# Kernel tuning notes

Measured on AMD Instinct MI355X. Metric: run time of the kernel, lower is better.

Reference implementation:

```python
import jax, jax.numpy as jnp
import numpy as np

N_NODES = 100000
IN_F = 512
OUT_F = 512
N_EDGES = 3200000


def setup_inputs() -> dict:
    key = jax.random.key(0)
    k1, k2, k3, k4, k5 = jax.random.split(key, 5)
    features = jax.random.normal(k1, (N_NODES, IN_F), dtype=jnp.float32)
    # xavier_uniform: bound = sqrt(6/(in+out))
    bound = np.sqrt(6.0 / (IN_F + OUT_F)).astype(np.float32)
    weight = jax.random.uniform(k2, (IN_F, OUT_F), dtype=jnp.float32,
                                minval=-bound, maxval=bound)
    edge_row = jax.random.randint(k3, (N_EDGES,), 0, N_NODES, dtype=jnp.int32)
    edge_col = jax.random.randint(k4, (N_EDGES,), 0, N_NODES, dtype=jnp.int32)
    # normalized-adjacency-like positive values
    edge_val = jax.random.uniform(k5, (N_EDGES,), dtype=jnp.float32)
    return {"features": features, "weight": weight, "edge_row": edge_row,
            "edge_col": edge_col, "edge_val": edge_val}


def reference(features, weight, edge_row, edge_col, edge_val):
    # support = features @ W   (dense GEMM, [N, out])
    support = features @ weight
    # output = spmm(adj, support): out[r] += val * support[c] for each edge (r, c)
    messages = edge_val[:, None] * support[edge_col]          # [E, out]
    output = jax.ops.segment_sum(messages, edge_row, num_segments=N_NODES)
    # active=True branch: fused ReLU
    return jax.nn.relu(output)
```

## Files before the change

### kernel.cpp

```cpp
#include <hip/hip_runtime.h>
#include <hip/hip_bf16.h>

#define N_NODES 100000
#define M_PAD   100096
#define FDIM    512
#define N_EDGES 3200000
#define GEMM_BLOCKS 3128
#define GEMM_MAIN   3104

#define NB    782
#define B1    782
#define SLICE 4096

typedef __attribute__((ext_vector_type(8))) short short8;
typedef __attribute__((ext_vector_type(8))) unsigned short ushort8;
typedef __attribute__((ext_vector_type(4))) float floatx4;
typedef __attribute__((ext_vector_type(2))) int intx2;

__device__ __forceinline__ unsigned short f2bf(float f) {
    unsigned u = __float_as_uint(f);
    u += 0x7FFFu + ((u >> 16) & 1u);
    return (unsigned short)(u >> 16);
}
__device__ __forceinline__ float bf2f(unsigned short u) {
    return __uint_as_float(((unsigned)u) << 16);
}

__global__ __launch_bounds__(256) void convert_w_k(const float* __restrict__ W,
                                                   unsigned short* __restrict__ Wt) {
    int idx = blockIdx.x * 256 + threadIdx.x;
    int k = idx >> 9, n = idx & 511;
    Wt[n * 512 + k] = f2bf(W[idx]);
}

__global__ __launch_bounds__(256) void convert_a_k(const float* __restrict__ F,
                                                   unsigned short* __restrict__ Af) {
    int i = blockIdx.x * 256 + threadIdx.x;
    if (i >= (N_NODES * FDIM) / 8) return;
    const float4* p = (const float4*)F + (size_t)i * 2;
    float4 a = p[0], b = p[1];
    ushort8 u = { f2bf(a.x), f2bf(a.y), f2bf(a.z), f2bf(a.w),
                  f2bf(b.x), f2bf(b.y), f2bf(b.z), f2bf(b.w) };
    *(ushort8*)(Af + (size_t)i * 8) = u;
}

__global__ __launch_bounds__(256) void hist1_k(const int* __restrict__ row,
                                               int* __restrict__ H) {
    __shared__ int h[NB];
    const int b = blockIdx.x;
    for (int k = threadIdx.x; k < NB; k += 256) h[k] = 0;
    __syncthreads();
    const int base = b * SLICE;
    const int limit = min(base + SLICE, N_EDGES);
    for (int i = base + threadIdx.x; i < limit; i += 256)
        atomicAdd(&h[row[i] >> 7], 1);
    __syncthreads();
    for (int k = threadIdx.x; k < NB; k += 256)
        H[b * NB + k] = h[k];
}

__global__ __launch_bounds__(1024) void scanA_k(int* __restrict__ H,
                                                int* __restrict__ totals) {
    __shared__ int sm[1024];
    const int k = blockIdx.x, tid = threadIdx.x;
    int v = (tid < B1) ? H[tid * NB + k] : 0;
    sm[tid] = v;
    __syncthreads();
    #pragma unroll
    for (int off = 1; off < 1024; off <<= 1) {
        int t = (tid >= off) ? sm[tid - off] : 0;
        __syncthreads();
        sm[tid] += t;
        __syncthreads();
    }
    if (tid < B1) H[tid * NB + k] = sm[tid] - v;
    if (tid == B1 - 1) totals[k] = sm[tid];
}

__global__ __launch_bounds__(1024) void scanB_k(const int* __restrict__ totals,
                                                int* __restrict__ start) {
    __shared__ int sm[1024];
    const int tid = threadIdx.x;
    int v = (tid < NB) ? totals[tid] : 0;
    sm[tid] = v;
    __syncthreads();
    #pragma unroll
    for (int off = 1; off < 1024; off <<= 1) {
        int t = (tid >= off) ? sm[tid - off] : 0;
        __syncthreads();
        sm[tid] += t;
        __syncthreads();
    }
    if (tid < NB) start[tid] = sm[tid] - v;
    if (tid == 0) start[NB] = N_EDGES;
}

__global__ __launch_bounds__(256) void scatter1_k(const int* __restrict__ row,
                                                  const int* __restrict__ col,
                                                  const float* __restrict__ val,
                                                  const int* __restrict__ H,
                                                  const int* __restrict__ start,
                                                  int2* __restrict__ tmp_cv,
                                                  unsigned char* __restrict__ tmp_r8) {
    __shared__ int cur[NB];
    const int b = blockIdx.x;
    for (int k = threadIdx.x; k < NB; k += 256)
        cur[k] = start[k] + H[b * NB + k];
    __syncthreads();
    const int base = b * SLICE;
    const int limit = min(base + SLICE, N_EDGES);
    for (int i = base + threadIdx.x; i < limit; i += 256) {
        int r = row[i];
        int p = atomicAdd(&cur[r >> 7], 1);
        tmp_cv[p] = make_int2(col[i], __float_as_int(val[i]));
        tmp_r8[p] = (unsigned char)(r & 127);
    }
}

__global__ __launch_bounds__(256) void sort2_k(const int* __restrict__ start,
                                               const int2* __restrict__ tmp_cv,
                                               const unsigned char* __restrict__ tmp_r8,
                                               int* __restrict__ row_start,
                                               int2* __restrict__ edges) {
    __shared__ int h[128];
    __shared__ int cur[128];
    const int k = blockIdx.x, tid = threadIdx.x;
    const int base = start[k], cnt = start[k + 1] - base;
    if (tid < 128) h[tid] = 0;
    __syncthreads();
    for (int i = tid; i < cnt; i += 256)
        atomicAdd(&h[tmp_r8[base + i]], 1);
    __syncthreads();
    int v = (tid < 128) ? h[tid] : 0;
    #pragma unroll
    for (int off = 1; off < 128; off <<= 1) {
        int t = (tid >= off && tid < 128) ? h[tid - off] : 0;
        __syncthreads();
        if (tid < 128) h[tid] += t;
        __syncthreads();
    }
    if (tid < 128) {
        int excl = h[tid] - v;
        int r = (k << 7) + tid;
        if (r < N_NODES) row_start[r] = base + excl;
        cur[tid] = base + excl;
    }
    if (k == NB - 1 && tid == 0) row_start[N_NODES] = N_EDGES;
    __syncthreads();
    for (int i = tid; i < cnt; i += 256) {
        unsigned char rl = tmp_r8[base + i];
        int p = atomicAdd(&cur[rl], 1);
        edges[p] = tmp_cv[base + i];
    }
}

__global__ __launch_bounds__(256) void gemm_k(const unsigned short* __restrict__ A,
                                              const unsigned short* __restrict__ Bt,
                                              unsigned short* __restrict__ C) {
    const int id = blockIdx.x;
    int mb, nb;
    if (id < GEMM_MAIN) {
        mb = (id >> 5) * 8 + (id & 7);
        nb = (id >> 3) & 3;
    } else {
        int t = id - GEMM_MAIN;
        mb = 776 + (t >> 2);
        nb = t & 3;
    }
    const int baseM = mb * 128;
    const int baseN = nb * 128;
    const int tid  = threadIdx.x;
    const int lane = tid & 63, wave = tid >> 6;
    const int wm = (wave & 1) * 64;
    const int wn = (wave >> 1) * 64;
    const int lrow = lane & 15, quad = lane >> 4;

    __shared__ unsigned short As[128 * 64];
    __shared__ unsigned short Bs[128 * 64];

    floatx4 acc[4][4] = {};

    for (int k0 = 0; k0 < FDIM; k0 += 64) {
        #pragma unroll
        for (int i = 0; i < 4; ++i) {
            int ofs = i * 4096 + tid * 16;
            int row = ofs >> 7;
            int ke  = (ofs & 127) >> 1;
            __builtin_amdgcn_global_load_lds(
                (const __attribute__((address_space(1))) void*)
                    (A + (size_t)(baseM + row) * FDIM + k0 + ke),
                (__attribute__((address_space(3))) void*)((char*)As + ofs),
                16, 0, 0);
            __builtin_amdgcn_global_load_lds(
                (const __attribute__((address_space(1))) void*)
                    (Bt + (size_t)(baseN + row) * FDIM + k0 + ke),
                (__attribute__((address_space(3))) void*)((char*)Bs + ofs),
                16, 0, 0);
        }
        __syncthreads();

        short8 af[4][2], bfr[4][2];
        #pragma unroll
        for (int mi = 0; mi < 4; ++mi)
            #pragma unroll
            for (int kk = 0; kk < 2; ++kk)
                af[mi][kk] = *(const short8*)(As + (wm + mi * 16 + lrow) * 64 + kk * 32 + quad * 8);
        #pragma unroll
        for (int ni = 0; ni < 4; ++ni)
            #pragma unroll
            for (int kk = 0; kk < 2; ++kk)
                bfr[ni][kk] = *(const short8*)(Bs + (wn + ni * 16 + lrow) * 64 + kk * 32 + quad * 8);
        #pragma unroll
        for (int kk = 0; kk < 2; ++kk)
            #pragma unroll
            for (int mi = 0; mi < 4; ++mi)
                #pragma unroll
                for (int ni = 0; ni < 4; ++ni)
                    acc[mi][ni] = __builtin_amdgcn_mfma_f32_16x16x32_bf16(
                        af[mi][kk], bfr[ni][kk], acc[mi][ni], 0, 0, 0);
        __syncthreads();
    }

    #pragma unroll
    for (int mi = 0; mi < 4; ++mi)
        #pragma unroll
        for (int ni = 0; ni < 4; ++ni)
            #pragma unroll
            for (int rr = 0; rr < 4; ++rr) {
                int row  = baseM + wm + mi * 16 + quad * 4 + rr;
                int colj = baseN + wn + ni * 16 + lrow;
                if (row < N_NODES)
                    C[(size_t)row * FDIM + colj] = f2bf(acc[mi][ni][rr]);
            }
}

__global__ __launch_bounds__(256) void spmm_k(const unsigned short* __restrict__ sup,
                                              const int* __restrict__ row_start,
                                              const int2* __restrict__ edges,
                                              float* __restrict__ out) {
    const int r = blockIdx.x * 4 + (threadIdx.x >> 6);
    const int lane = threadIdx.x & 63;
    const int start = row_start[r], end = row_start[r + 1];
    const unsigned short* supl = sup + lane * 8;

    float acc[8] = {0.f, 0.f, 0.f, 0.f, 0.f, 0.f, 0.f, 0.f};

    const int n8 = (end - start) & ~7;
    for (int eb = start; eb < start + n8; eb += 8) {
        intx2 p[8];
        #pragma unroll
        for (int j = 0; j < 8; ++j)
            p[j] = __builtin_nontemporal_load((const intx2*)&edges[eb + j]);
        ushort8 s[8];
        #pragma unroll
        for (int j = 0; j < 8; ++j)
            s[j] = *(const ushort8*)(supl + (size_t)p[j].x * FDIM);
        #pragma unroll
        for (int j = 0; j < 8; ++j) {
            float v = __int_as_float(p[j].y);
            #pragma unroll
            for (int i = 0; i < 8; ++i)
                acc[i] += v * bf2f((unsigned short)s[j][i]);
        }
    }
    for (int e = start + n8; e < end; ++e) {
        intx2 p = __builtin_nontemporal_load((const intx2*)&edges[e]);
        ushort8 s = *(const ushort8*)(supl + (size_t)p.x * FDIM);
        float v = __int_as_float(p.y);
        #pragma unroll
        for (int i = 0; i < 8; ++i) acc[i] += v * bf2f((unsigned short)s[i]);
    }

    float* op = out + (size_t)r * FDIM + lane * 8;
    floatx4 o0 = { fmaxf(acc[0], 0.f), fmaxf(acc[1], 0.f),
                   fmaxf(acc[2], 0.f), fmaxf(acc[3], 0.f) };
    floatx4 o1 = { fmaxf(acc[4], 0.f), fmaxf(acc[5], 0.f),
                   fmaxf(acc[6], 0.f), fmaxf(acc[7], 0.f) };
    __builtin_nontemporal_store(o0, (floatx4*)op);
    __builtin_nontemporal_store(o1, (floatx4*)(op + 4));
}

extern "C" void kernel_launch(void* const* d_in, const int* in_sizes, int n_in,
                              void* d_out, int out_size, void* d_ws, size_t ws_size,
                              hipStream_t stream) {
    const float* features = (const float*)d_in[0];
    const float* weight   = (const float*)d_in[1];
    const int*   edge_row = (const int*)d_in[2];
    const int*   edge_col = (const int*)d_in[3];
    const float* edge_val = (const float*)d_in[4];
    float* out = (float*)d_out;

    char* ws = (char*)d_ws;
    size_t off = 0;
    unsigned short* sup = (unsigned short*)(ws + off); off += (size_t)N_NODES * FDIM * 2;
    unsigned short* Af  = (unsigned short*)(ws + off); off += (size_t)M_PAD * FDIM * 2;
    unsigned short* Wt  = (unsigned short*)(ws + off); off += (size_t)FDIM * FDIM * 2;
    int* row_start = (int*)(ws + off); off += 400128;
    int2* edges    = (int2*)(ws + off); off += (size_t)N_EDGES * 8;
    char* supb = (char*)sup;
    int2* tmp_cv          = (int2*)(supb);
    unsigned char* tmp_r8 = (unsigned char*)(supb + 25600000);
    int* H      = (int*)(supb + 28800000);
    int* totals = (int*)(supb + 31246336);
    int* startb = (int*)(supb + 31250432);

    convert_w_k<<<dim3((FDIM * FDIM) / 256), dim3(256), 0, stream>>>(weight, Wt);
    convert_a_k<<<dim3((N_NODES * FDIM / 8 + 255) / 256), dim3(256), 0, stream>>>(features, Af);
    hist1_k<<<dim3(B1), dim3(256), 0, stream>>>(edge_row, H);
    scanA_k<<<dim3(NB), dim3(1024), 0, stream>>>(H, totals);
    scanB_k<<<dim3(1), dim3(1024), 0, stream>>>(totals, startb);
    scatter1_k<<<dim3(B1), dim3(256), 0, stream>>>(edge_row, edge_col, edge_val,
                                                   H, startb, tmp_cv, tmp_r8);
    sort2_k<<<dim3(NB), dim3(256), 0, stream>>>(startb, tmp_cv, tmp_r8, row_start, edges);
    gemm_k<<<dim3(GEMM_BLOCKS), dim3(256), 0, stream>>>(Af, Wt, sup);
    spmm_k<<<dim3(N_NODES / 4), dim3(256), 0, stream>>>(sup, row_start, edges, out);
}
```

Baseline: 1.101 ms.

## Widen sort buckets to 256 rows and stage GEMM epilogue through LDS

The two-level bucket sort now uses 391 coarse buckets of 256 rows instead of 782 of 128. That halves the histogram matrix the column scans touch and gives the per-bucket sort kernel full 256-thread use. The GEMM epilogue now writes each 16-row slab of accumulators to shared memory and then stores 16-byte vectors to global memory, replacing scattered 2-byte stores. This adds extra barriers and LDS traffic in the epilogue, and each sort2 block now handles about twice as many edges.

```diff
diff --git a/kernel.cpp b/kernel.cpp
--- a/kernel.cpp
+++ b/kernel.cpp
@@ -8,7 +8,7 @@
 #define GEMM_BLOCKS 3128
 #define GEMM_MAIN   3104
 
-#define NB    782
+#define NB    391
 #define B1    782
 #define SLICE 4096
 
@@ -53,7 +53,7 @@
     const int base = b * SLICE;
     const int limit = min(base + SLICE, N_EDGES);
     for (int i = base + threadIdx.x; i < limit; i += 256)
-        atomicAdd(&h[row[i] >> 7], 1);
+        atomicAdd(&h[row[i] >> 8], 1);
     __syncthreads();
     for (int k = threadIdx.x; k < NB; k += 256)
         H[b * NB + k] = h[k];
@@ -77,15 +77,15 @@
     if (tid == B1 - 1) totals[k] = sm[tid];
 }
 
-__global__ __launch_bounds__(1024) void scanB_k(const int* __restrict__ totals,
-                                                int* __restrict__ start) {
-    __shared__ int sm[1024];
+__global__ __launch_bounds__(512) void scanB_k(const int* __restrict__ totals,
+                                               int* __restrict__ start) {
+    __shared__ int sm[512];
     const int tid = threadIdx.x;
     int v = (tid < NB) ? totals[tid] : 0;
     sm[tid] = v;
     __syncthreads();
     #pragma unroll
-    for (int off = 1; off < 1024; off <<= 1) {
+    for (int off = 1; off < 512; off <<= 1) {
         int t = (tid >= off) ? sm[tid - off] : 0;
         __syncthreads();
         sm[tid] += t;
@@ -111,9 +111,9 @@
     const int limit = min(base + SLICE, N_EDGES);
     for (int i = base + threadIdx.x; i < limit; i += 256) {
         int r = row[i];
-        int p = atomicAdd(&cur[r >> 7], 1);
+        int p = atomicAdd(&cur[r >> 8], 1);
         tmp_cv[p] = make_int2(col[i], __float_as_int(val[i]));
-        tmp_r8[p] = (unsigned char)(r & 127);
+        tmp_r8[p] = (unsigned char)(r & 255);
     }
 }
 
@@ -122,29 +122,27 @@
                                                const unsigned char* __restrict__ tmp_r8,
                                                int* __restrict__ row_start,
                                                int2* __restrict__ edges) {
-    __shared__ int h[128];
-    __shared__ int cur[128];
+    __shared__ int h[256];
+    __shared__ int cur[256];
     const int k = blockIdx.x, tid = threadIdx.x;
     const int base = start[k], cnt = start[k + 1] - base;
-    if (tid < 128) h[tid] = 0;
+    h[tid] = 0;
     __syncthreads();
     for (int i = tid; i < cnt; i += 256)
         atomicAdd(&h[tmp_r8[base + i]], 1);
     __syncthreads();
-    int v = (tid < 128) ? h[tid] : 0;
+    int v = h[tid];
     #pragma unroll
-    for (int off = 1; off < 128; off <<= 1) {
-        int t = (tid >= off && tid < 128) ? h[tid - off] : 0;
-        __syncthreads();
-        if (tid < 128) h[tid] += t;
-        __syncthreads();
-    }
-    if (tid < 128) {
-        int excl = h[tid] - v;
-        int r = (k << 7) + tid;
-        if (r < N_NODES) row_start[r] = base + excl;
-        cur[tid] = base + excl;
-    }
+    for (int off = 1; off < 256; off <<= 1) {
+        int t = (tid >= off) ? h[tid - off] : 0;
+        __syncthreads();
+        h[tid] += t;
+        __syncthreads();
+    }
+    int excl = h[tid] - v;
+    int r = (k << 8) + tid;
+    if (r < N_NODES) row_start[r] = base + excl;
+    cur[tid] = base + excl;
     if (k == NB - 1 && tid == 0) row_start[N_NODES] = N_EDGES;
     __syncthreads();
     for (int i = tid; i < cnt; i += 256) {
@@ -221,17 +219,28 @@
         __syncthreads();
     }
 
+    unsigned short* Ls = Bs;
+    const int erow = (wave & 1) * 16 + quad * 4;
     #pragma unroll
-    for (int mi = 0; mi < 4; ++mi)
+    for (int mi = 0; mi < 4; ++mi) {
+        __syncthreads();
         #pragma unroll
         for (int ni = 0; ni < 4; ++ni)
             #pragma unroll
-            for (int rr = 0; rr < 4; ++rr) {
-                int row  = baseM + wm + mi * 16 + quad * 4 + rr;
-                int colj = baseN + wn + ni * 16 + lrow;
-                if (row < N_NODES)
-                    C[(size_t)row * FDIM + colj] = f2bf(acc[mi][ni][rr]);
+            for (int rr = 0; rr < 4; ++rr)
+                Ls[(erow + rr) * 136 + wn + ni * 16 + lrow] = f2bf(acc[mi][ni][rr]);
+        __syncthreads();
+        #pragma unroll
+        for (int it = 0; it < 2; ++it) {
+            int q  = tid + it * 256;
+            int rl = q >> 4;
+            int gr = baseM + ((rl & 16) ? 64 : 0) + mi * 16 + (rl & 15);
+            if (gr < N_NODES) {
+                uint4 v = *(const uint4*)(Ls + rl * 136 + (q & 15) * 8);
+                *(uint4*)(C + (size_t)gr * FDIM + baseN + (q & 15) * 8) = v;
             }
+        }
+    }
 }
 
 __global__ __launch_bounds__(256) void spmm_k(const unsigned short* __restrict__ sup,
@@ -301,14 +310,14 @@
     int2* tmp_cv          = (int2*)(supb);
     unsigned char* tmp_r8 = (unsigned char*)(supb + 25600000);
     int* H      = (int*)(supb + 28800000);
-    int* totals = (int*)(supb + 31246336);
-    int* startb = (int*)(supb + 31250432);
+    int* totals = (int*)(supb + 30026240);
+    int* startb = (int*)(supb + 30030336);
 
     convert_w_k<<<dim3((FDIM * FDIM) / 256), dim3(256), 0, stream>>>(weight, Wt);
     convert_a_k<<<dim3((N_NODES * FDIM / 8 + 255) / 256), dim3(256), 0, stream>>>(features, Af);
     hist1_k<<<dim3(B1), dim3(256), 0, stream>>>(edge_row, H);
     scanA_k<<<dim3(NB), dim3(1024), 0, stream>>>(H, totals);
-    scanB_k<<<dim3(1), dim3(1024), 0, stream>>>(totals, startb);
+    scanB_k<<<dim3(1), dim3(512), 0, stream>>>(totals, startb);
     scatter1_k<<<dim3(B1), dim3(256), 0, stream>>>(edge_row, edge_col, edge_val,
                                                    H, startb, tmp_cv, tmp_r8);
     sort2_k<<<dim3(NB), dim3(256), 0, stream>>>(startb, tmp_cv, tmp_r8, row_start, edges);
```

Result: faster. 1.069 ms (-2.9%).
